# Optimization experiments

Hardware: AMD Instinct MI355X
Metric: run time of the kernel (lower is better)

Reference implementation:

```python
import jax, jax.numpy as jnp
import numpy as np

B, S, H, DH = 2, 4096, 8, 64
D = H * DH


def setup_inputs() -> dict:
    key = jax.random.key(0)
    ks = jax.random.split(key, 6)
    std = 1.0 / np.sqrt(D)
    return {
        "x": jax.random.normal(ks[0], (B, S, D), dtype=jnp.float32),
        "Wq": jax.random.normal(ks[1], (D, D), dtype=jnp.float32) * std,
        "Wk": jax.random.normal(ks[2], (D, D), dtype=jnp.float32) * std,
        "Wv": jax.random.normal(ks[3], (D, D), dtype=jnp.float32) * std,
        "Wo": jax.random.normal(ks[4], (D, D), dtype=jnp.float32) * std,
        "bo": jnp.zeros((D,), dtype=jnp.float32),
    }


def reference(x, Wq, Wk, Wv, Wo, bo):
    scale = DH ** (-0.5)
    # torch Linear: y = x @ W.T
    q = x @ Wq.T  # [B,S,D]
    k = x @ Wk.T
    v = x @ Wv.T
    # split heads -> [B,H,S,Dh]
    q = q.reshape(B, S, H, DH).transpose(0, 2, 1, 3)
    k = k.reshape(B, S, H, DH).transpose(0, 2, 1, 3)
    v = v.reshape(B, S, H, DH).transpose(0, 2, 1, 3)
    score = jnp.einsum('bhqd,bhkd->bhqk', q, k) * scale  # [B,H,S,S]
    weights = jax.nn.softmax(score, axis=-1)
    attn = jnp.einsum('bhqk,bhkd->bhqd', weights, v)  # [B,H,S,Dh]
    h_ = attn.transpose(0, 2, 1, 3).reshape(B, S, D)
    return h_ @ Wo.T + bo
```

## Files before the change

### kernel.cpp

```cpp
#include <hip/hip_runtime.h>

#define LOG2E 1.44269504088896340736f

typedef unsigned short u16;
typedef __bf16 bf16x4_t __attribute__((ext_vector_type(4)));
typedef __bf16 bf16x8_t __attribute__((ext_vector_type(8)));
typedef float f32x4_t __attribute__((ext_vector_type(4)));

__device__ __forceinline__ f32x4_t mfma16(bf16x8_t a, bf16x8_t b, f32x4_t c) {
  return __builtin_amdgcn_mfma_f32_16x16x32_bf16(a, b, c, 0, 0, 0);
}

__device__ __forceinline__ void gl_lds16(const u16* g, u16* l) {
  __builtin_amdgcn_global_load_lds(
      (const __attribute__((address_space(1))) unsigned int*)g,
      (__attribute__((address_space(3))) unsigned int*)l, 16, 0, 0);
}

__device__ __forceinline__ void cvt_store(u16* dst, f32x4_t a, f32x4_t b, float scale) {
  a *= scale; b *= scale;
  union { uint4 u; struct { bf16x4_t lo, hi; } s; } c;
  c.s.lo = __builtin_convertvector(a, bf16x4_t);
  c.s.hi = __builtin_convertvector(b, bf16x4_t);
  *(uint4*)dst = c.u;
}

template <int MODE>
__device__ __forceinline__ void gemm_core_f32(const float* __restrict__ A, const float* __restrict__ Bt,
                                              u16* __restrict__ Cout, int Mbase, int Nbase,
                                              float bscale) {
  __shared__ __align__(16) u16 As[128][40];
  __shared__ __align__(16) u16 Bs[128][40];
  const int t = threadIdx.x;
  const int wave = t >> 6, lane = t & 63;
  const int r = lane & 15, qd = lane >> 4;
  const int wm = wave & 1, wn = wave >> 1;
  const int lr = t >> 2;
  const int lc = (t & 3) * 8;

  f32x4_t acc[4][4];
#pragma unroll
  for (int i = 0; i < 4; i++)
#pragma unroll
    for (int j = 0; j < 4; j++) { f32x4_t z = {0.f, 0.f, 0.f, 0.f}; acc[i][j] = z; }

  const float* pa0 = A  + (Mbase + lr) * 512 + lc;
  const float* pa1 = A  + (Mbase + 64 + lr) * 512 + lc;
  const float* pb0 = Bt + (Nbase + lr) * 512 + lc;
  const float* pb1 = Bt + (Nbase + 64 + lr) * 512 + lc;

  f32x4_t ra0[2], ra1[2], rb0[2], rb1[2];
  ra0[0] = *(const f32x4_t*)(pa0); ra0[1] = *(const f32x4_t*)(pa0 + 4);
  ra1[0] = *(const f32x4_t*)(pa1); ra1[1] = *(const f32x4_t*)(pa1 + 4);
  rb0[0] = *(const f32x4_t*)(pb0); rb0[1] = *(const f32x4_t*)(pb0 + 4);
  rb1[0] = *(const f32x4_t*)(pb1); rb1[1] = *(const f32x4_t*)(pb1 + 4);

  for (int k0 = 0; k0 < 512; k0 += 32) {
    cvt_store(&As[lr][lc],      ra0[0], ra0[1], 1.f);
    cvt_store(&As[64 + lr][lc], ra1[0], ra1[1], 1.f);
    cvt_store(&Bs[lr][lc],      rb0[0], rb0[1], bscale);
    cvt_store(&Bs[64 + lr][lc], rb1[0], rb1[1], bscale);
    __syncthreads();
    if (k0 < 480) {
      ra0[0] = *(const f32x4_t*)(pa0 + k0 + 32); ra0[1] = *(const f32x4_t*)(pa0 + k0 + 36);
      ra1[0] = *(const f32x4_t*)(pa1 + k0 + 32); ra1[1] = *(const f32x4_t*)(pa1 + k0 + 36);
      rb0[0] = *(const f32x4_t*)(pb0 + k0 + 32); rb0[1] = *(const f32x4_t*)(pb0 + k0 + 36);
      rb1[0] = *(const f32x4_t*)(pb1 + k0 + 32); rb1[1] = *(const f32x4_t*)(pb1 + k0 + 36);
    }
    bf16x8_t af[4], bfr[4];
#pragma unroll
    for (int i = 0; i < 4; i++) af[i]  = *(const bf16x8_t*)&As[wm * 64 + i * 16 + r][qd * 8];
#pragma unroll
    for (int j = 0; j < 4; j++) bfr[j] = *(const bf16x8_t*)&Bs[wn * 64 + j * 16 + r][qd * 8];
#pragma unroll
    for (int i = 0; i < 4; i++)
#pragma unroll
      for (int j = 0; j < 4; j++) acc[i][j] = mfma16(af[i], bfr[j], acc[i][j]);
    __syncthreads();
  }

#pragma unroll
  for (int i = 0; i < 4; i++) {
#pragma unroll
    for (int reg = 0; reg < 4; reg++) {
      int gr = Mbase + wm * 64 + i * 16 + qd * 4 + reg;
#pragma unroll
      for (int j = 0; j < 4; j++) {
        int gc = Nbase + wn * 64 + j * 16 + r;
        float val = acc[i][j][reg];
        if (MODE == 1) {
          int bb = gc >> 12, ss = gc & 4095;
          ((__bf16*)Cout)[((long)(bb * 512 + gr)) * 4096 + ss] = (__bf16)val;
        } else {
          ((__bf16*)Cout)[gr * 512 + gc] = (__bf16)val;
        }
      }
    }
  }
}

__global__ __launch_bounds__(256) void gemm_qkv_kernel(
    const float* __restrict__ X,
    const float* __restrict__ Wq, const float* __restrict__ Wk, const float* __restrict__ Wv,
    u16* __restrict__ Q, u16* __restrict__ K, u16* __restrict__ Vt) {
  if (blockIdx.z == 0)
    gemm_core_f32<0>(X, Wq, Q, blockIdx.x * 128, blockIdx.y * 128, 0.125f * LOG2E);
  else if (blockIdx.z == 1)
    gemm_core_f32<0>(X, Wk, K, blockIdx.x * 128, blockIdx.y * 128, 1.f);
  else
    gemm_core_f32<1>(Wv, X, Vt, blockIdx.y * 128, blockIdx.x * 128, 1.f);
}

__global__ __launch_bounds__(256) void gemm_out_kernel(
    const u16* __restrict__ Aat, const float* __restrict__ Wo,
    float* __restrict__ Out, const float* __restrict__ bo) {
  __shared__ __align__(16) u16 As[64][40];
  __shared__ __align__(16) u16 Bs[128][40];
  const int t = threadIdx.x;
  const int wave = t >> 6, lane = t & 63;
  const int r = lane & 15, qd = lane >> 4;
  const int wn = wave;
  const int Mbase = blockIdx.x * 64, Nbase = blockIdx.y * 128;
  const int lr = t >> 2;
  const int lc = (t & 3) * 8;

  f32x4_t acc[4][2];
#pragma unroll
  for (int i = 0; i < 4; i++)
#pragma unroll
    for (int j = 0; j < 2; j++) { f32x4_t z = {0.f, 0.f, 0.f, 0.f}; acc[i][j] = z; }

  const u16*  pa  = Aat + (Mbase + lr) * 512 + lc;
  const float* pb0 = Wo + (Nbase + lr) * 512 + lc;
  const float* pb1 = Wo + (Nbase + 64 + lr) * 512 + lc;

  uint4 ra = *(const uint4*)(pa);
  f32x4_t rb0[2], rb1[2];
  rb0[0] = *(const f32x4_t*)(pb0); rb0[1] = *(const f32x4_t*)(pb0 + 4);
  rb1[0] = *(const f32x4_t*)(pb1); rb1[1] = *(const f32x4_t*)(pb1 + 4);

  for (int k0 = 0; k0 < 512; k0 += 32) {
    *(uint4*)&As[lr][lc] = ra;
    cvt_store(&Bs[lr][lc],      rb0[0], rb0[1], 1.f);
    cvt_store(&Bs[64 + lr][lc], rb1[0], rb1[1], 1.f);
    __syncthreads();
    if (k0 < 480) {
      ra = *(const uint4*)(pa + k0 + 32);
      rb0[0] = *(const f32x4_t*)(pb0 + k0 + 32); rb0[1] = *(const f32x4_t*)(pb0 + k0 + 36);
      rb1[0] = *(const f32x4_t*)(pb1 + k0 + 32); rb1[1] = *(const f32x4_t*)(pb1 + k0 + 36);
    }
    bf16x8_t af[4], bfr[2];
#pragma unroll
    for (int i = 0; i < 4; i++) af[i]  = *(const bf16x8_t*)&As[i * 16 + r][qd * 8];
#pragma unroll
    for (int j = 0; j < 2; j++) bfr[j] = *(const bf16x8_t*)&Bs[wn * 32 + j * 16 + r][qd * 8];
#pragma unroll
    for (int i = 0; i < 4; i++)
#pragma unroll
      for (int j = 0; j < 2; j++) acc[i][j] = mfma16(af[i], bfr[j], acc[i][j]);
    __syncthreads();
  }

  float bv[2];
#pragma unroll
  for (int j = 0; j < 2; j++) bv[j] = bo[Nbase + wn * 32 + j * 16 + r];
#pragma unroll
  for (int i = 0; i < 4; i++)
#pragma unroll
    for (int reg = 0; reg < 4; reg++) {
      int gr = Mbase + i * 16 + qd * 4 + reg;
#pragma unroll
      for (int j = 0; j < 2; j++) {
        int gc = Nbase + wn * 32 + j * 16 + r;
        Out[gr * 512 + gc] = acc[i][j][reg] + bv[j];
      }
    }
}

__global__ __launch_bounds__(256, 2) void attn_kernel(
    const u16* __restrict__ Q, const u16* __restrict__ K, const u16* __restrict__ Vt,
    u16* __restrict__ Oattn) {
  __shared__ __align__(16) u16 Ks[2][2][4096];
  __shared__ __align__(16) u16 Vs[2][2][4096];

  const int t = threadIdx.x;
  const int wave = t >> 6, lane = t & 63;
  const int r = lane & 15, qd = lane >> 4;
  const int g = wave & 1, kv = wave >> 1;
  const int bh = blockIdx.y;
  const int b = bh >> 3, h = bh & 7;
  const long bbase = (long)b * 4096 * 512;
  const int q0 = blockIdx.x * 128;

  const int sw = r & 7;
  const int ck0 = (qd ^ sw) * 8;
  const int ck1 = ((qd + 4) ^ sw) * 8;
  int vo0[2], vo1[2];
#pragma unroll
  for (int c = 0; c < 2; c++) {
    vo0[c] = ((c * 4 + (qd >> 1)) ^ sw) * 8 + 4 * (qd & 1);
    vo1[c] = ((c * 4 + 2 + (qd >> 1)) ^ sw) * 8 + 4 * (qd & 1);
  }

  bf16x8_t ones8;
#pragma unroll
  for (int j = 0; j < 8; j++) ones8[j] = (__bf16)1.0f;

  bf16x8_t qf[4][2];
#pragma unroll
  for (int qa = 0; qa < 4; qa++) {
    const u16* qp = Q + bbase + (long)(q0 + g * 64 + qa * 16 + r) * 512 + h * 64 + qd * 8;
    qf[qa][0] = *(const bf16x8_t*)(qp);
    qf[qa][1] = *(const bf16x8_t*)(qp + 32);
  }

  f32x4_t accO[4][4];
  f32x4_t accL[4];
#pragma unroll
  for (int qa = 0; qa < 4; qa++) {
    f32x4_t z = {0.f, 0.f, 0.f, 0.f};
    accL[qa] = z;
#pragma unroll
    for (int nt = 0; nt < 4; nt++) accO[qa][nt] = z;
  }

  const int rr = lane >> 3;
  const int cc = (lane & 7) ^ rr;
  const u16* kgb = K + bbase + (long)(kv * 2048 + g * 32 + rr) * 512 + h * 64 + cc * 8;
  const u16* vgb = Vt + ((long)(b * 512 + h * 64 + g * 32 + rr)) * 4096 + kv * 2048 + cc * 8;

#pragma unroll
  for (int i = 0; i < 4; i++) gl_lds16(kgb + (long)i * 8 * 512, &Ks[kv][0][g * 2048] + i * 512);
#pragma unroll
  for (int i = 0; i < 4; i++) gl_lds16(vgb + i * 8 * 4096, &Vs[kv][0][g * 2048] + i * 512);

  for (int it = 0; it < 32; it++) {
    const int buf = it & 1;
    __syncthreads();

    if (it < 31) {
      const int nb = (it + 1) & 1;
      const long ko = (long)(it + 1) * 64;
#pragma unroll
      for (int i = 0; i < 4; i++)
        gl_lds16(kgb + (ko + i * 8) * 512, &Ks[kv][nb][g * 2048] + i * 512);
#pragma unroll
      for (int i = 0; i < 4; i++)
        gl_lds16(vgb + ko + (long)i * 8 * 4096, &Vs[kv][nb][g * 2048] + i * 512);
    }

    bf16x8_t kf[4][2];
#pragma unroll
    for (int nt = 0; nt < 4; nt++) {
      const u16* kb = &Ks[kv][buf][(nt * 16 + r) * 64];
      kf[nt][0] = *(const bf16x8_t*)(kb + ck0);
      kf[nt][1] = *(const bf16x8_t*)(kb + ck1);
    }

    f32x4_t St[4][4];
#pragma unroll
    for (int qa = 0; qa < 4; qa++)
#pragma unroll
      for (int nt = 0; nt < 4; nt++) {
        f32x4_t z = {0.f, 0.f, 0.f, 0.f};
        z = mfma16(kf[nt][0], qf[qa][0], z);
        z = mfma16(kf[nt][1], qf[qa][1], z);
        St[qa][nt] = z;
      }

    bf16x8_t pf[4][2];
#pragma unroll
    for (int qa = 0; qa < 4; qa++)
#pragma unroll
      for (int c = 0; c < 2; c++) {
        f32x4_t e0, e1;
#pragma unroll
        for (int j = 0; j < 4; j++) {
          e0[j] = __builtin_amdgcn_exp2f(St[qa][2 * c][j]);
          e1[j] = __builtin_amdgcn_exp2f(St[qa][2 * c + 1][j]);
        }
        bf16x4_t b0 = __builtin_convertvector(e0, bf16x4_t);
        bf16x4_t b1 = __builtin_convertvector(e1, bf16x4_t);
        bf16x8_t p8;
#pragma unroll
        for (int j = 0; j < 4; j++) { p8[j] = b0[j]; p8[4 + j] = b1[j]; }
        pf[qa][c] = p8;
      }

#pragma unroll
    for (int qa = 0; qa < 4; qa++)
#pragma unroll
      for (int c = 0; c < 2; c++)
        accL[qa] = mfma16(ones8, pf[qa][c], accL[qa]);

#pragma unroll
    for (int c = 0; c < 2; c++) {
      bf16x8_t va[4];
#pragma unroll
      for (int dm = 0; dm < 4; dm++) {
        const u16* vb = &Vs[kv][buf][(dm * 16 + r) * 64];
        union { uint4 u; bf16x8_t v; } cat;
        *(uint2*)&cat.u.x = *(const uint2*)(vb + vo0[c]);
        *(uint2*)&cat.u.z = *(const uint2*)(vb + vo1[c]);
        va[dm] = cat.v;
      }
#pragma unroll
      for (int qa = 0; qa < 4; qa++)
#pragma unroll
        for (int dm = 0; dm < 4; dm++)
          accO[qa][dm] = mfma16(va[dm], pf[qa][c], accO[qa][dm]);
    }
  }

  __syncthreads();
  float* Sc  = (float*)&Ks[0][0][0];
  float* Lsc = (float*)&Vs[0][0][0];
  if (kv == 1) {
#pragma unroll
    for (int qa = 0; qa < 4; qa++) {
#pragma unroll
      for (int dm = 0; dm < 4; dm++)
        *(f32x4_t*)&Sc[g * 4096 + ((qa * 4 + dm) * 64 + lane) * 4] = accO[qa][dm];
      Lsc[g * 256 + qa * 64 + lane] = accL[qa][0];
    }
  }
  __syncthreads();
  if (kv == 0) {
#pragma unroll
    for (int qa = 0; qa < 4; qa++) {
      float L = accL[qa][0] + Lsc[g * 256 + qa * 64 + lane];
      float inv = 1.f / L;
      int gq = q0 + g * 64 + qa * 16 + r;
#pragma unroll
      for (int dm = 0; dm < 4; dm++) {
        f32x4_t o = *(const f32x4_t*)&Sc[g * 4096 + ((qa * 4 + dm) * 64 + lane) * 4];
        o += accO[qa][dm];
        bf16x4_t ob;
#pragma unroll
        for (int reg = 0; reg < 4; reg++) ob[reg] = (__bf16)(o[reg] * inv);
        *(uint2*)&Oattn[bbase + (long)gq * 512 + h * 64 + dm * 16 + qd * 4] = *(uint2*)&ob;
      }
    }
  }
}

extern "C" void kernel_launch(void* const* d_in, const int* in_sizes, int n_in,
                              void* d_out, int out_size, void* d_ws, size_t ws_size,
                              hipStream_t stream) {
  const float* x  = (const float*)d_in[0];
  const float* Wq = (const float*)d_in[1];
  const float* Wk = (const float*)d_in[2];
  const float* Wv = (const float*)d_in[3];
  const float* Wo = (const float*)d_in[4];
  const float* bo = (const float*)d_in[5];
  float* out = (float*)d_out;

  u16* ws  = (u16*)d_ws;
  u16* Qb  = ws;
  u16* Kb  = Qb  + 4194304;
  u16* Vtg = Kb  + 4194304;
  u16* Ab  = Vtg + 4194304;

  dim3 g1(64, 4, 3);
  gemm_qkv_kernel<<<g1, 256, 0, stream>>>(x, Wq, Wk, Wv, Qb, Kb, Vtg);

  dim3 g2(32, 16);
  attn_kernel<<<g2, 256, 0, stream>>>(Qb, Kb, Vtg, Ab);

  dim3 g3(128, 4);
  gemm_out_kernel<<<g3, 256, 0, stream>>>(Ab, Wo, out, bo);
}
```

Before: 187.7 us.

## Fuse Q/K/V projections into one block sharing X tiles with LDS-staged stores

Replaces the three-way z-split QKV GEMM with one kernel per (64-token, 128-feature) tile. Each tile computes Q and K together from a shared X tile, then computes V transposed. Outputs are staged through LDS so global writes are coalesced 16-byte stores, replacing the scattered per-element bf16 stores; this matters most for the transposed V layout. The change trades more sequential work per block and larger LDS use (unioned) for fewer X re-reads and better store coalescing. X is still loaded twice per block, once for the Q/K pass and once for the V pass.

```diff
diff --git a/kernel.cpp b/kernel.cpp
--- a/kernel.cpp
+++ b/kernel.cpp
@@ -25,90 +25,171 @@
   *(uint4*)dst = c.u;
 }
 
-template <int MODE>
-__device__ __forceinline__ void gemm_core_f32(const float* __restrict__ A, const float* __restrict__ Bt,
-                                              u16* __restrict__ Cout, int Mbase, int Nbase,
-                                              float bscale) {
-  __shared__ __align__(16) u16 As[128][40];
-  __shared__ __align__(16) u16 Bs[128][40];
+__global__ __launch_bounds__(256, 2) void proj_kernel(
+    const float* __restrict__ X, const float* __restrict__ Wq,
+    const float* __restrict__ Wk, const float* __restrict__ Wv,
+    u16* __restrict__ Q, u16* __restrict__ K, u16* __restrict__ Vt) {
+  __shared__ __align__(16) union {
+    struct { u16 A[64 * 40]; u16 Bq[128 * 40]; u16 Bk[128 * 40]; } qk;
+    struct { u16 Av[128 * 40]; u16 Bx[64 * 40]; } v;
+    u16 T2[64 * 136];
+    u16 T[128 * 72];
+  } sh;
+
   const int t = threadIdx.x;
   const int wave = t >> 6, lane = t & 63;
   const int r = lane & 15, qd = lane >> 4;
-  const int wm = wave & 1, wn = wave >> 1;
+  const int hm = wave & 1, wn = wave >> 1;
+  const int tokBase = blockIdx.x * 64;
+  const int featBase = blockIdx.y * 128;
   const int lr = t >> 2;
   const int lc = (t & 3) * 8;
 
-  f32x4_t acc[4][4];
+  const float* pA  = X  + (tokBase + lr) * 512 + lc;
+  const float* pq0 = Wq + (featBase + lr) * 512 + lc;
+  const float* pq1 = Wq + (featBase + 64 + lr) * 512 + lc;
+  const float* pk0 = Wk + (featBase + lr) * 512 + lc;
+  const float* pk1 = Wk + (featBase + 64 + lr) * 512 + lc;
+
+  f32x4_t rA[2], rq0[2], rq1[2], rk0[2], rk1[2];
+  rA[0]  = *(const f32x4_t*)(pA);  rA[1]  = *(const f32x4_t*)(pA + 4);
+  rq0[0] = *(const f32x4_t*)(pq0); rq0[1] = *(const f32x4_t*)(pq0 + 4);
+  rq1[0] = *(const f32x4_t*)(pq1); rq1[1] = *(const f32x4_t*)(pq1 + 4);
+  rk0[0] = *(const f32x4_t*)(pk0); rk0[1] = *(const f32x4_t*)(pk0 + 4);
+  rk1[0] = *(const f32x4_t*)(pk1); rk1[1] = *(const f32x4_t*)(pk1 + 4);
+
+  f32x4_t accq[2][4], acck[2][4];
+#pragma unroll
+  for (int i = 0; i < 2; i++)
+#pragma unroll
+    for (int j = 0; j < 4; j++) {
+      f32x4_t z = {0.f, 0.f, 0.f, 0.f};
+      accq[i][j] = z; acck[i][j] = z;
+    }
+
+  const float qsc = 0.125f * LOG2E;
+  for (int k0 = 0; k0 < 512; k0 += 32) {
+    cvt_store(&sh.qk.A[lr * 40 + lc],         rA[0],  rA[1],  1.f);
+    cvt_store(&sh.qk.Bq[lr * 40 + lc],        rq0[0], rq0[1], qsc);
+    cvt_store(&sh.qk.Bq[(64 + lr) * 40 + lc], rq1[0], rq1[1], qsc);
+    cvt_store(&sh.qk.Bk[lr * 40 + lc],        rk0[0], rk0[1], 1.f);
+    cvt_store(&sh.qk.Bk[(64 + lr) * 40 + lc], rk1[0], rk1[1], 1.f);
+    __syncthreads();
+    if (k0 < 480) {
+      rA[0]  = *(const f32x4_t*)(pA  + k0 + 32); rA[1]  = *(const f32x4_t*)(pA  + k0 + 36);
+      rq0[0] = *(const f32x4_t*)(pq0 + k0 + 32); rq0[1] = *(const f32x4_t*)(pq0 + k0 + 36);
+      rq1[0] = *(const f32x4_t*)(pq1 + k0 + 32); rq1[1] = *(const f32x4_t*)(pq1 + k0 + 36);
+      rk0[0] = *(const f32x4_t*)(pk0 + k0 + 32); rk0[1] = *(const f32x4_t*)(pk0 + k0 + 36);
+      rk1[0] = *(const f32x4_t*)(pk1 + k0 + 32); rk1[1] = *(const f32x4_t*)(pk1 + k0 + 36);
+    }
+    bf16x8_t af[2], bq[4], bk[4];
+#pragma unroll
+    for (int i = 0; i < 2; i++) af[i] = *(const bf16x8_t*)&sh.qk.A[(hm * 32 + i * 16 + r) * 40 + qd * 8];
+#pragma unroll
+    for (int j = 0; j < 4; j++) {
+      bq[j] = *(const bf16x8_t*)&sh.qk.Bq[(wn * 64 + j * 16 + r) * 40 + qd * 8];
+      bk[j] = *(const bf16x8_t*)&sh.qk.Bk[(wn * 64 + j * 16 + r) * 40 + qd * 8];
+    }
+#pragma unroll
+    for (int i = 0; i < 2; i++)
+#pragma unroll
+      for (int j = 0; j < 4; j++) {
+        accq[i][j] = mfma16(af[i], bq[j], accq[i][j]);
+        acck[i][j] = mfma16(af[i], bk[j], acck[i][j]);
+      }
+    __syncthreads();
+  }
+
+  const float* pv0 = Wv + (featBase + lr) * 512 + lc;
+  const float* pv1 = Wv + (featBase + 64 + lr) * 512 + lc;
+  f32x4_t rv0[2], rv1[2], rx[2];
+  rv0[0] = *(const f32x4_t*)(pv0); rv0[1] = *(const f32x4_t*)(pv0 + 4);
+  rv1[0] = *(const f32x4_t*)(pv1); rv1[1] = *(const f32x4_t*)(pv1 + 4);
+  rx[0]  = *(const f32x4_t*)(pA);  rx[1]  = *(const f32x4_t*)(pA + 4);
+
+#pragma unroll
+  for (int i = 0; i < 2; i++)
+#pragma unroll
+    for (int j = 0; j < 4; j++)
+#pragma unroll
+      for (int reg = 0; reg < 4; reg++)
+        *(__bf16*)&sh.T2[(hm * 32 + i * 16 + qd * 4 + reg) * 136 + wn * 64 + j * 16 + r] =
+            (__bf16)accq[i][j][reg];
+  __syncthreads();
+#pragma unroll
+  for (int rd = 0; rd < 4; rd++) {
+    int row = (t >> 4) + rd * 16;
+    int c = (t & 15) * 8;
+    uint4 val = *(const uint4*)&sh.T2[row * 136 + c];
+    *(uint4*)&Q[(long)(tokBase + row) * 512 + featBase + c] = val;
+  }
+  __syncthreads();
+
+#pragma unroll
+  for (int i = 0; i < 2; i++)
+#pragma unroll
+    for (int j = 0; j < 4; j++)
+#pragma unroll
+      for (int reg = 0; reg < 4; reg++)
+        *(__bf16*)&sh.T2[(hm * 32 + i * 16 + qd * 4 + reg) * 136 + wn * 64 + j * 16 + r] =
+            (__bf16)acck[i][j][reg];
+  __syncthreads();
+#pragma unroll
+  for (int rd = 0; rd < 4; rd++) {
+    int row = (t >> 4) + rd * 16;
+    int c = (t & 15) * 8;
+    uint4 val = *(const uint4*)&sh.T2[row * 136 + c];
+    *(uint4*)&K[(long)(tokBase + row) * 512 + featBase + c] = val;
+  }
+  __syncthreads();
+
+  f32x4_t accv[4][2];
 #pragma unroll
   for (int i = 0; i < 4; i++)
 #pragma unroll
-    for (int j = 0; j < 4; j++) { f32x4_t z = {0.f, 0.f, 0.f, 0.f}; acc[i][j] = z; }
-
-  const float* pa0 = A  + (Mbase + lr) * 512 + lc;
-  const float* pa1 = A  + (Mbase + 64 + lr) * 512 + lc;
-  const float* pb0 = Bt + (Nbase + lr) * 512 + lc;
-  const float* pb1 = Bt + (Nbase + 64 + lr) * 512 + lc;
-
-  f32x4_t ra0[2], ra1[2], rb0[2], rb1[2];
-  ra0[0] = *(const f32x4_t*)(pa0); ra0[1] = *(const f32x4_t*)(pa0 + 4);
-  ra1[0] = *(const f32x4_t*)(pa1); ra1[1] = *(const f32x4_t*)(pa1 + 4);
-  rb0[0] = *(const f32x4_t*)(pb0); rb0[1] = *(const f32x4_t*)(pb0 + 4);
-  rb1[0] = *(const f32x4_t*)(pb1); rb1[1] = *(const f32x4_t*)(pb1 + 4);
+    for (int j = 0; j < 2; j++) { f32x4_t z = {0.f, 0.f, 0.f, 0.f}; accv[i][j] = z; }
 
   for (int k0 = 0; k0 < 512; k0 += 32) {
-    cvt_store(&As[lr][lc],      ra0[0], ra0[1], 1.f);
-    cvt_store(&As[64 + lr][lc], ra1[0], ra1[1], 1.f);
-    cvt_store(&Bs[lr][lc],      rb0[0], rb0[1], bscale);
-    cvt_store(&Bs[64 + lr][lc], rb1[0], rb1[1], bscale);
+    cvt_store(&sh.v.Av[lr * 40 + lc],         rv0[0], rv0[1], 1.f);
+    cvt_store(&sh.v.Av[(64 + lr) * 40 + lc],  rv1[0], rv1[1], 1.f);
+    cvt_store(&sh.v.Bx[lr * 40 + lc],         rx[0],  rx[1],  1.f);
     __syncthreads();
     if (k0 < 480) {
-      ra0[0] = *(const f32x4_t*)(pa0 + k0 + 32); ra0[1] = *(const f32x4_t*)(pa0 + k0 + 36);
-      ra1[0] = *(const f32x4_t*)(pa1 + k0 + 32); ra1[1] = *(const f32x4_t*)(pa1 + k0 + 36);
-      rb0[0] = *(const f32x4_t*)(pb0 + k0 + 32); rb0[1] = *(const f32x4_t*)(pb0 + k0 + 36);
-      rb1[0] = *(const f32x4_t*)(pb1 + k0 + 32); rb1[1] = *(const f32x4_t*)(pb1 + k0 + 36);
-    }
-    bf16x8_t af[4], bfr[4];
-#pragma unroll
-    for (int i = 0; i < 4; i++) af[i]  = *(const bf16x8_t*)&As[wm * 64 + i * 16 + r][qd * 8];
-#pragma unroll
-    for (int j = 0; j < 4; j++) bfr[j] = *(const bf16x8_t*)&Bs[wn * 64 + j * 16 + r][qd * 8];
+      rv0[0] = *(const f32x4_t*)(pv0 + k0 + 32); rv0[1] = *(const f32x4_t*)(pv0 + k0 + 36);
+      rv1[0] = *(const f32x4_t*)(pv1 + k0 + 32); rv1[1] = *(const f32x4_t*)(pv1 + k0 + 36);
+      rx[0]  = *(const f32x4_t*)(pA  + k0 + 32); rx[1]  = *(const f32x4_t*)(pA  + k0 + 36);
+    }
+    bf16x8_t av[4], bx[2];
+#pragma unroll
+    for (int i = 0; i < 4; i++) av[i] = *(const bf16x8_t*)&sh.v.Av[(hm * 64 + i * 16 + r) * 40 + qd * 8];
+#pragma unroll
+    for (int j = 0; j < 2; j++) bx[j] = *(const bf16x8_t*)&sh.v.Bx[(wn * 32 + j * 16 + r) * 40 + qd * 8];
 #pragma unroll
     for (int i = 0; i < 4; i++)
 #pragma unroll
-      for (int j = 0; j < 4; j++) acc[i][j] = mfma16(af[i], bfr[j], acc[i][j]);
-    __syncthreads();
-  }
-
-#pragma unroll
-  for (int i = 0; i < 4; i++) {
-#pragma unroll
-    for (int reg = 0; reg < 4; reg++) {
-      int gr = Mbase + wm * 64 + i * 16 + qd * 4 + reg;
-#pragma unroll
-      for (int j = 0; j < 4; j++) {
-        int gc = Nbase + wn * 64 + j * 16 + r;
-        float val = acc[i][j][reg];
-        if (MODE == 1) {
-          int bb = gc >> 12, ss = gc & 4095;
-          ((__bf16*)Cout)[((long)(bb * 512 + gr)) * 4096 + ss] = (__bf16)val;
-        } else {
-          ((__bf16*)Cout)[gr * 512 + gc] = (__bf16)val;
-        }
-      }
-    }
-  }
-}
-
-__global__ __launch_bounds__(256) void gemm_qkv_kernel(
-    const float* __restrict__ X,
-    const float* __restrict__ Wq, const float* __restrict__ Wk, const float* __restrict__ Wv,
-    u16* __restrict__ Q, u16* __restrict__ K, u16* __restrict__ Vt) {
-  if (blockIdx.z == 0)
-    gemm_core_f32<0>(X, Wq, Q, blockIdx.x * 128, blockIdx.y * 128, 0.125f * LOG2E);
-  else if (blockIdx.z == 1)
-    gemm_core_f32<0>(X, Wk, K, blockIdx.x * 128, blockIdx.y * 128, 1.f);
-  else
-    gemm_core_f32<1>(Wv, X, Vt, blockIdx.y * 128, blockIdx.x * 128, 1.f);
+      for (int j = 0; j < 2; j++) accv[i][j] = mfma16(av[i], bx[j], accv[i][j]);
+    __syncthreads();
+  }
+
+#pragma unroll
+  for (int i = 0; i < 4; i++)
+#pragma unroll
+    for (int j = 0; j < 2; j++)
+#pragma unroll
+      for (int reg = 0; reg < 4; reg++)
+        *(__bf16*)&sh.T[(hm * 64 + i * 16 + qd * 4 + reg) * 72 + wn * 32 + j * 16 + r] =
+            (__bf16)accv[i][j][reg];
+  __syncthreads();
+  {
+    const int bb = tokBase >> 12, ss = tokBase & 4095;
+#pragma unroll
+    for (int rd = 0; rd < 4; rd++) {
+      int f = (t >> 3) + rd * 32;
+      int c = (t & 7) * 8;
+      uint4 val = *(const uint4*)&sh.T[f * 72 + c];
+      *(uint4*)&Vt[((long)(bb * 512 + featBase + f)) * 4096 + ss + c] = val;
+    }
+  }
 }
 
 __global__ __launch_bounds__(256) void gemm_out_kernel(
@@ -130,7 +211,7 @@
 #pragma unroll
     for (int j = 0; j < 2; j++) { f32x4_t z = {0.f, 0.f, 0.f, 0.f}; acc[i][j] = z; }
 
-  const u16*  pa  = Aat + (Mbase + lr) * 512 + lc;
+  const u16*   pa  = Aat + (Mbase + lr) * 512 + lc;
   const float* pb0 = Wo + (Nbase + lr) * 512 + lc;
   const float* pb1 = Wo + (Nbase + 64 + lr) * 512 + lc;
 
@@ -361,8 +442,8 @@
   u16* Vtg = Kb  + 4194304;
   u16* Ab  = Vtg + 4194304;
 
-  dim3 g1(64, 4, 3);
-  gemm_qkv_kernel<<<g1, 256, 0, stream>>>(x, Wq, Wk, Wv, Qb, Kb, Vtg);
+  dim3 g1(128, 4);
+  proj_kernel<<<g1, 256, 0, stream>>>(x, Wq, Wk, Wv, Qb, Kb, Vtg);
 
   dim3 g2(32, 16);
   attn_kernel<<<g2, 256, 0, stream>>>(Qb, Kb, Vtg, Ab);
```

New measurement: 190.2 us. Within noise of the previous version (+1.3%).
